# Performance work log

Hardware: AMD Instinct MI355X
Metric: run time of the kernel (lower is better)

## Reference

```python
import jax, jax.numpy as jnp
import numpy as np

D_DIST = 1.5       # init kwarg d_dist
NUM_LABELS = 64    # K; labels drawn from [0, K), all present w.h.p. at N=200k
B, C, N = 8, 32, 200000


def setup_inputs() -> dict:
    key = jax.random.key(0)
    k1, k2 = jax.random.split(key)
    prediction = jax.random.normal(k1, (B, C, N), dtype=jnp.float32)
    label = jax.random.randint(k2, (B, N), 0, NUM_LABELS)
    return {"prediction": prediction, "label": label}


def _batch_loss(pred, lab):
    # pred: [C, N], lab: [N] int in [0, K)
    K = NUM_LABELS
    counts = jax.ops.segment_sum(jnp.ones(lab.shape, pred.dtype), lab, num_segments=K)  # [K]
    sums = jax.ops.segment_sum(pred.T, lab, num_segments=K)                              # [K, C]
    center = sums / jnp.maximum(counts, 1.0)[:, None]                                    # [K, C] per-label mean
    # square_distance_single(center, center): pairwise sq-dist between the C columns
    # of center (coordinates are the K cluster axes) -> [C, C], exactly as the torch code.
    gram = center.T @ center                       # [C, C]
    n2 = jnp.sum(center * center, axis=0)          # [C]
    sq = jax.nn.relu(n2[:, None] + n2[None, :] - 2.0 * gram)
    # safe sqrt: identical forward to sqrt(relu(sq)) but finite grads at 0
    dist = jnp.where(sq > 0, jnp.sqrt(jnp.where(sq > 0, sq, 1.0)), 0.0)
    hinge = jax.nn.relu(2.0 * D_DIST - dist)
    return jnp.sum(hinge * hinge) / (2.0 * K * (K - 1.0 + 1e-16))


def reference(prediction, label):
    # sum over batches, matching the python loop accumulation
    return jnp.sum(jax.vmap(_batch_loss)(prediction, label))
```

## Files before the change

kernel.cpp:

```cpp
#include <hip/hip_runtime.h>
#include <stdint.h>

#define BATCH    8
#define CDIM     32
#define KLBL     64
#define NPB      200000
#define SLABS_PB 6250
#define CHUNKS   128
#define TSLAB    4
#define LROWB    272
#define TILEB    (32 * LROWB)

typedef __attribute__((ext_vector_type(8))) short bf16x8;
typedef __attribute__((ext_vector_type(4))) float f32x4;

union ABits { uint32_t u[4]; bf16x8 v; };

__device__ __forceinline__ uint32_t cvtpk_bf16(float lo, float hi) {
  uint32_t r;
  asm volatile("v_cvt_pk_bf16_f32 %0, %1, %2" : "=v"(r) : "v"(lo), "v"(hi));
  return r;
}

__global__ __launch_bounds__(256) void pack_kernel(
    const int* __restrict__ lab, uint8_t* __restrict__ lab8, int total4) {
  const int i = blockIdx.x * 256 + threadIdx.x;
  if (i < total4) {
    const int4 l4 = ((const int4*)lab)[i];
    ((uint32_t*)lab8)[i] = (uint32_t)(l4.x & 0xff) |
                           ((uint32_t)(l4.y & 0xff) << 8) |
                           ((uint32_t)(l4.z & 0xff) << 16) |
                           ((uint32_t)(l4.w & 0xff) << 24);
  }
}

__global__ __launch_bounds__(256) void seg_mfma_kernel(
    const float* __restrict__ pred,
    const uint8_t* __restrict__ lab8,
    float* __restrict__ gsums,
    float* __restrict__ gcounts) {
  __shared__ __align__(8)  uint32_t s_lab[400];
  __shared__ __align__(16) uint8_t  s_tile[2][TILEB];

  const int tid = threadIdx.x;
  const int wv = tid >> 6;
  const int ln = tid & 63;
  const int chunk = blockIdx.x, b = blockIdx.y;

  const int s0 = (int)((long long)chunk * SLABS_PB / CHUNKS);
  const int s1 = (int)((long long)(chunk + 1) * SLABS_PB / CHUNKS);
  const int nslab = s1 - s0;
  const int base_n = s0 * 32;

  const uint32_t* lsrc = (const uint32_t*)(lab8 + (size_t)b * NPB + base_n);
  for (int i = tid; i < nslab * 8; i += 256) s_lab[i] = lsrc[i];

  const float* rowp[4];
#pragma unroll
  for (int j = 0; j < 4; ++j) {
    const int c = wv * 8 + j * 2 + (ln >> 5);
    rowp[j] = pred + ((size_t)b * CDIM + c) * NPB;
  }
  const int lan4 = (ln & 31) * 4;

  ABits ones;
  ones.u[0] = ones.u[1] = ones.u[2] = ones.u[3] = 0x3F803F80u;

  f32x4 acc0 = {0.f, 0.f, 0.f, 0.f};
  f32x4 acc1 = {0.f, 0.f, 0.f, 0.f};
  f32x4 accc = {0.f, 0.f, 0.f, 0.f};

  const int ntile = (nslab + TSLAB - 1) / TSLAB;
  const uint32_t myrow = (uint32_t)((ln & 15) + (wv << 4));

  float4 r0, r1, r2, r3;

  auto issue_loads = [&](int t) {
    int en = base_n + t * 128 + lan4;
    en = min(en, NPB - 4);
    r0 = *(const float4*)(rowp[0] + en);
    r1 = *(const float4*)(rowp[1] + en);
    r2 = *(const float4*)(rowp[2] + en);
    r3 = *(const float4*)(rowp[3] + en);
  };

  auto cvt_write = [&](int buf) {
    uint8_t* tb = s_tile[buf];
    const int off = (ln & 31) * 8;
#pragma unroll
    for (int j = 0; j < 4; ++j) {
      const float4 r = (j == 0) ? r0 : (j == 1) ? r1 : (j == 2) ? r2 : r3;
      const int c = wv * 8 + j * 2 + (ln >> 5);
      uint2 w;
      w.x = cvtpk_bf16(r.x, r.y);
      w.y = cvtpk_bf16(r.z, r.w);
      *(uint2*)(tb + c * LROWB + off) = w;
    }
  };

  auto process = [&](int t, int buf) {
    const uint8_t* tb = s_tile[buf];
    const int ns = min(TSLAB, nslab - t * TSLAB);
    const int rb = (ln & 15) * LROWB + (ln >> 4) * 16;
    for (int ss = 0; ss < ns; ++ss) {
      const int sb = t * TSLAB + ss;
      const uint2 lw =
          *(const uint2*)((const uint8_t*)s_lab + sb * 32 + (ln >> 4) * 8);
      ABits a;
      a.u[0] = (((lw.x) & 0xffu) == myrow ? 0x3F80u : 0u) |
               (((lw.x >> 8) & 0xffu) == myrow ? 0x3F800000u : 0u);
      a.u[1] = (((lw.x >> 16) & 0xffu) == myrow ? 0x3F80u : 0u) |
               (((lw.x >> 24) & 0xffu) == myrow ? 0x3F800000u : 0u);
      a.u[2] = (((lw.y) & 0xffu) == myrow ? 0x3F80u : 0u) |
               (((lw.y >> 8) & 0xffu) == myrow ? 0x3F800000u : 0u);
      a.u[3] = (((lw.y >> 16) & 0xffu) == myrow ? 0x3F80u : 0u) |
               (((lw.y >> 24) & 0xffu) == myrow ? 0x3F800000u : 0u);
      const bf16x8 b0 = *(const bf16x8*)(tb + rb + ss * 64);
      const bf16x8 b1 = *(const bf16x8*)(tb + rb + ss * 64 + 16 * LROWB);
      acc0 = __builtin_amdgcn_mfma_f32_16x16x32_bf16(a.v, b0, acc0, 0, 0, 0);
      acc1 = __builtin_amdgcn_mfma_f32_16x16x32_bf16(a.v, b1, acc1, 0, 0, 0);
      accc = __builtin_amdgcn_mfma_f32_16x16x32_bf16(a.v, ones.v, accc, 0, 0, 0);
    }
  };

  issue_loads(0);
  cvt_write(0);
  __syncthreads();

  for (int t = 0; t < ntile; ++t) {
    const int buf = t & 1;
    const bool more = (t + 1 < ntile);
    if (more) issue_loads(t + 1);
    __builtin_amdgcn_sched_barrier(0);
    process(t, buf);
    if (more) cvt_write(buf ^ 1);
    __syncthreads();
  }

  const int krb = (wv << 4) + ((ln >> 4) << 2);
  const int col = ln & 15;
  float* gs = gsums + (size_t)b * KLBL * CDIM;
#pragma unroll
  for (int r = 0; r < 4; ++r) {
    atomicAdd(&gs[(krb + r) * CDIM + col], acc0[r]);
    atomicAdd(&gs[(krb + r) * CDIM + 16 + col], acc1[r]);
  }
  if (col == 0) {
#pragma unroll
    for (int r = 0; r < 4; ++r)
      atomicAdd(&gcounts[b * KLBL + krb + r], accc[r]);
  }
}

__global__ __launch_bounds__(256) void loss_kernel(
    const float* __restrict__ gsums,
    const float* __restrict__ gcounts,
    float* __restrict__ out) {
  const int b = blockIdx.x;
  __shared__ float s_center[KLBL * CDIM];
  __shared__ float s_red[256];

  for (int i = threadIdx.x; i < KLBL * CDIM; i += 256) {
    const float cnt = fmaxf(gcounts[b * KLBL + (i >> 5)], 1.0f);
    s_center[i] = gsums[(size_t)b * KLBL * CDIM + i] / cnt;
  }
  __syncthreads();

  float acc = 0.f;
  for (int p = threadIdx.x; p < CDIM * CDIM; p += 256) {
    const int i = p >> 5, j = p & 31;
    float g = 0.f, ni = 0.f, nj = 0.f;
#pragma unroll
    for (int k = 0; k < KLBL; ++k) {
      const float ci = s_center[k * CDIM + i];
      const float cj = s_center[k * CDIM + j];
      g += ci * cj;
      ni += ci * ci;
      nj += cj * cj;
    }
    float sq = fmaxf(ni + nj - 2.f * g, 0.f);
    const float dist = (sq > 0.f) ? sqrtf(sq) : 0.f;
    const float h = fmaxf(3.0f - dist, 0.f);
    acc += h * h;
  }

  s_red[threadIdx.x] = acc;
  __syncthreads();
  for (int s = 128; s > 0; s >>= 1) {
    if (threadIdx.x < s) s_red[threadIdx.x] += s_red[threadIdx.x + s];
    __syncthreads();
  }
  if (threadIdx.x == 0)
    atomicAdd(out, s_red[0] / (2.0f * (float)KLBL * ((float)KLBL - 1.0f)));
}

extern "C" void kernel_launch(void* const* d_in, const int* in_sizes, int n_in,
                              void* d_out, int out_size, void* d_ws, size_t ws_size,
                              hipStream_t stream) {
  const float* pred  = (const float*)d_in[0];
  const int*   label = (const int*)d_in[1];
  float* out = (float*)d_out;

  float*   gsums   = (float*)d_ws;
  float*   gcounts = gsums + (size_t)BATCH * KLBL * CDIM;
  uint8_t* lab8    = (uint8_t*)(gcounts + BATCH * KLBL);

  const size_t accum_bytes =
      (size_t)(BATCH * KLBL * CDIM + BATCH * KLBL) * sizeof(float);
  hipMemsetAsync(d_ws, 0, accum_bytes, stream);
  hipMemsetAsync(d_out, 0, sizeof(float), stream);

  const int total4 = BATCH * NPB / 4;
  pack_kernel<<<(total4 + 255) / 256, 256, 0, stream>>>(label, lab8, total4);

  dim3 grid1(CHUNKS, BATCH);
  seg_mfma_kernel<<<grid1, 256, 0, stream>>>(pred, lab8, gsums, gcounts);

  loss_kernel<<<BATCH, 256, 0, stream>>>(gsums, gcounts, out);
}
```

Baseline: 68.44 us.

## Fuse label packing into segment kernel and deepen prefetch to two tiles

```diff
diff --git a/kernel.cpp b/kernel.cpp
--- a/kernel.cpp
+++ b/kernel.cpp
@@ -22,21 +22,9 @@
   return r;
 }
 
-__global__ __launch_bounds__(256) void pack_kernel(
-    const int* __restrict__ lab, uint8_t* __restrict__ lab8, int total4) {
-  const int i = blockIdx.x * 256 + threadIdx.x;
-  if (i < total4) {
-    const int4 l4 = ((const int4*)lab)[i];
-    ((uint32_t*)lab8)[i] = (uint32_t)(l4.x & 0xff) |
-                           ((uint32_t)(l4.y & 0xff) << 8) |
-                           ((uint32_t)(l4.z & 0xff) << 16) |
-                           ((uint32_t)(l4.w & 0xff) << 24);
-  }
-}
-
 __global__ __launch_bounds__(256) void seg_mfma_kernel(
     const float* __restrict__ pred,
-    const uint8_t* __restrict__ lab8,
+    const int*   __restrict__ label,
     float* __restrict__ gsums,
     float* __restrict__ gcounts) {
   __shared__ __align__(8)  uint32_t s_lab[400];
@@ -52,8 +40,12 @@
   const int nslab = s1 - s0;
   const int base_n = s0 * 32;
 
-  const uint32_t* lsrc = (const uint32_t*)(lab8 + (size_t)b * NPB + base_n);
-  for (int i = tid; i < nslab * 8; i += 256) s_lab[i] = lsrc[i];
+  const int4* lsrc = (const int4*)(label + (size_t)b * NPB + base_n);
+  for (int i = tid; i < nslab * 8; i += 256) {
+    const int4 l4 = lsrc[i];
+    s_lab[i] = (uint32_t)(l4.x & 0xff) | ((uint32_t)(l4.y & 0xff) << 8) |
+               ((uint32_t)(l4.z & 0xff) << 16) | ((uint32_t)(l4.w & 0xff) << 24);
+  }
 
   const float* rowp[4];
 #pragma unroll
@@ -73,28 +65,47 @@
   const int ntile = (nslab + TSLAB - 1) / TSLAB;
   const uint32_t myrow = (uint32_t)((ln & 15) + (wv << 4));
 
-  float4 r0, r1, r2, r3;
-
-  auto issue_loads = [&](int t) {
-    int en = base_n + t * 128 + lan4;
-    en = min(en, NPB - 4);
-    r0 = *(const float4*)(rowp[0] + en);
-    r1 = *(const float4*)(rowp[1] + en);
-    r2 = *(const float4*)(rowp[2] + en);
-    r3 = *(const float4*)(rowp[3] + en);
-  };
-
-  auto cvt_write = [&](int buf) {
+  float4 rA0, rA1, rA2, rA3;
+  float4 rB0, rB1, rB2, rB3;
+
+  auto loadA = [&](int t) {
+    const int en = min(base_n + t * 128 + lan4, NPB - 4);
+    rA0 = *(const float4*)(rowp[0] + en);
+    rA1 = *(const float4*)(rowp[1] + en);
+    rA2 = *(const float4*)(rowp[2] + en);
+    rA3 = *(const float4*)(rowp[3] + en);
+  };
+  auto loadB = [&](int t) {
+    const int en = min(base_n + t * 128 + lan4, NPB - 4);
+    rB0 = *(const float4*)(rowp[0] + en);
+    rB1 = *(const float4*)(rowp[1] + en);
+    rB2 = *(const float4*)(rowp[2] + en);
+    rB3 = *(const float4*)(rowp[3] + en);
+  };
+
+  const int cvt_off = (ln & 31) * 8;
+  auto cvtA = [&](int buf) {
     uint8_t* tb = s_tile[buf];
-    const int off = (ln & 31) * 8;
 #pragma unroll
     for (int j = 0; j < 4; ++j) {
-      const float4 r = (j == 0) ? r0 : (j == 1) ? r1 : (j == 2) ? r2 : r3;
+      const float4 r = (j == 0) ? rA0 : (j == 1) ? rA1 : (j == 2) ? rA2 : rA3;
       const int c = wv * 8 + j * 2 + (ln >> 5);
       uint2 w;
       w.x = cvtpk_bf16(r.x, r.y);
       w.y = cvtpk_bf16(r.z, r.w);
-      *(uint2*)(tb + c * LROWB + off) = w;
+      *(uint2*)(tb + c * LROWB + cvt_off) = w;
+    }
+  };
+  auto cvtB = [&](int buf) {
+    uint8_t* tb = s_tile[buf];
+#pragma unroll
+    for (int j = 0; j < 4; ++j) {
+      const float4 r = (j == 0) ? rB0 : (j == 1) ? rB1 : (j == 2) ? rB2 : rB3;
+      const int c = wv * 8 + j * 2 + (ln >> 5);
+      uint2 w;
+      w.x = cvtpk_bf16(r.x, r.y);
+      w.y = cvtpk_bf16(r.z, r.w);
+      *(uint2*)(tb + c * LROWB + cvt_off) = w;
     }
   };
 
@@ -123,18 +134,26 @@
     }
   };
 
-  issue_loads(0);
-  cvt_write(0);
+  loadA(0);
+  if (ntile > 1) loadB(1);
+  cvtA(0);
   __syncthreads();
 
-  for (int t = 0; t < ntile; ++t) {
-    const int buf = t & 1;
-    const bool more = (t + 1 < ntile);
-    if (more) issue_loads(t + 1);
+  int t = 0;
+  while (t < ntile) {
+    if (t + 2 < ntile) loadA(t + 2);
     __builtin_amdgcn_sched_barrier(0);
-    process(t, buf);
-    if (more) cvt_write(buf ^ 1);
+    process(t, 0);
+    if (t + 1 < ntile) cvtB(1);
     __syncthreads();
+    ++t;
+    if (t >= ntile) break;
+    if (t + 2 < ntile) loadB(t + 2);
+    __builtin_amdgcn_sched_barrier(0);
+    process(t, 1);
+    if (t + 1 < ntile) cvtA(0);
+    __syncthreads();
+    ++t;
   }
 
   const int krb = (wv << 4) + ((ln >> 4) << 2);
@@ -201,20 +220,16 @@
   const int*   label = (const int*)d_in[1];
   float* out = (float*)d_out;
 
-  float*   gsums   = (float*)d_ws;
-  float*   gcounts = gsums + (size_t)BATCH * KLBL * CDIM;
-  uint8_t* lab8    = (uint8_t*)(gcounts + BATCH * KLBL);
+  float* gsums   = (float*)d_ws;
+  float* gcounts = gsums + (size_t)BATCH * KLBL * CDIM;
 
   const size_t accum_bytes =
       (size_t)(BATCH * KLBL * CDIM + BATCH * KLBL) * sizeof(float);
   hipMemsetAsync(d_ws, 0, accum_bytes, stream);
   hipMemsetAsync(d_out, 0, sizeof(float), stream);
 
-  const int total4 = BATCH * NPB / 4;
-  pack_kernel<<<(total4 + 255) / 256, 256, 0, stream>>>(label, lab8, total4);
-
   dim3 grid1(CHUNKS, BATCH);
-  seg_mfma_kernel<<<grid1, 256, 0, stream>>>(pred, lab8, gsums, gcounts);
+  seg_mfma_kernel<<<grid1, 256, 0, stream>>>(pred, label, gsums, gcounts);
 
   loss_kernel<<<BATCH, 256, 0, stream>>>(gsums, gcounts, out);
 }
```

After: 66.33 us. -3.1%, faster.

## Load pred and labels directly into MFMA registers, drop pack kernel and LDS tiles

Applied to the files above, without the earlier changes.

```diff
diff --git a/kernel.cpp b/kernel.cpp
--- a/kernel.cpp
+++ b/kernel.cpp
@@ -6,10 +6,7 @@
 #define KLBL     64
 #define NPB      200000
 #define SLABS_PB 6250
-#define CHUNKS   128
-#define TSLAB    4
-#define LROWB    272
-#define TILEB    (32 * LROWB)
+#define CHUNKS   96
 
 typedef __attribute__((ext_vector_type(8))) short bf16x8;
 typedef __attribute__((ext_vector_type(4))) float f32x4;
@@ -22,25 +19,12 @@
   return r;
 }
 
-__global__ __launch_bounds__(256) void pack_kernel(
-    const int* __restrict__ lab, uint8_t* __restrict__ lab8, int total4) {
-  const int i = blockIdx.x * 256 + threadIdx.x;
-  if (i < total4) {
-    const int4 l4 = ((const int4*)lab)[i];
-    ((uint32_t*)lab8)[i] = (uint32_t)(l4.x & 0xff) |
-                           ((uint32_t)(l4.y & 0xff) << 8) |
-                           ((uint32_t)(l4.z & 0xff) << 16) |
-                           ((uint32_t)(l4.w & 0xff) << 24);
-  }
-}
-
 __global__ __launch_bounds__(256) void seg_mfma_kernel(
     const float* __restrict__ pred,
-    const uint8_t* __restrict__ lab8,
+    const int*   __restrict__ label,
     float* __restrict__ gsums,
     float* __restrict__ gcounts) {
-  __shared__ __align__(8)  uint32_t s_lab[400];
-  __shared__ __align__(16) uint8_t  s_tile[2][TILEB];
+  __shared__ float s_part[4][KLBL * CDIM + KLBL];
 
   const int tid = threadIdx.x;
   const int wv = tid >> 6;
@@ -49,106 +33,116 @@
 
   const int s0 = (int)((long long)chunk * SLABS_PB / CHUNKS);
   const int s1 = (int)((long long)(chunk + 1) * SLABS_PB / CHUNKS);
-  const int nslab = s1 - s0;
-  const int base_n = s0 * 32;
-
-  const uint32_t* lsrc = (const uint32_t*)(lab8 + (size_t)b * NPB + base_n);
-  for (int i = tid; i < nslab * 8; i += 256) s_lab[i] = lsrc[i];
-
-  const float* rowp[4];
-#pragma unroll
-  for (int j = 0; j < 4; ++j) {
-    const int c = wv * 8 + j * 2 + (ln >> 5);
-    rowp[j] = pred + ((size_t)b * CDIM + c) * NPB;
-  }
-  const int lan4 = (ln & 31) * 4;
+  const int w0 = s0 + (int)((long long)(s1 - s0) * wv / 4);
+  const int w1 = s0 + (int)((long long)(s1 - s0) * (wv + 1) / 4);
+
+  const int crow = ln & 15;
+  const int kseg = (ln >> 4) * 8;
+
+  const float* row0 = pred + ((size_t)b * CDIM + crow) * NPB;
+  const float* row1 = pred + ((size_t)b * CDIM + crow + 16) * NPB;
+  const int*   labp = label + (size_t)b * NPB;
 
   ABits ones;
   ones.u[0] = ones.u[1] = ones.u[2] = ones.u[3] = 0x3F803F80u;
 
-  f32x4 acc0 = {0.f, 0.f, 0.f, 0.f};
-  f32x4 acc1 = {0.f, 0.f, 0.f, 0.f};
-  f32x4 accc = {0.f, 0.f, 0.f, 0.f};
-
-  const int ntile = (nslab + TSLAB - 1) / TSLAB;
-  const uint32_t myrow = (uint32_t)((ln & 15) + (wv << 4));
-
-  float4 r0, r1, r2, r3;
-
-  auto issue_loads = [&](int t) {
-    int en = base_n + t * 128 + lan4;
-    en = min(en, NPB - 4);
-    r0 = *(const float4*)(rowp[0] + en);
-    r1 = *(const float4*)(rowp[1] + en);
-    r2 = *(const float4*)(rowp[2] + en);
-    r3 = *(const float4*)(rowp[3] + en);
-  };
-
-  auto cvt_write = [&](int buf) {
-    uint8_t* tb = s_tile[buf];
-    const int off = (ln & 31) * 8;
-#pragma unroll
-    for (int j = 0; j < 4; ++j) {
-      const float4 r = (j == 0) ? r0 : (j == 1) ? r1 : (j == 2) ? r2 : r3;
-      const int c = wv * 8 + j * 2 + (ln >> 5);
-      uint2 w;
-      w.x = cvtpk_bf16(r.x, r.y);
-      w.y = cvtpk_bf16(r.z, r.w);
-      *(uint2*)(tb + c * LROWB + off) = w;
-    }
-  };
-
-  auto process = [&](int t, int buf) {
-    const uint8_t* tb = s_tile[buf];
-    const int ns = min(TSLAB, nslab - t * TSLAB);
-    const int rb = (ln & 15) * LROWB + (ln >> 4) * 16;
-    for (int ss = 0; ss < ns; ++ss) {
-      const int sb = t * TSLAB + ss;
-      const uint2 lw =
-          *(const uint2*)((const uint8_t*)s_lab + sb * 32 + (ln >> 4) * 8);
-      ABits a;
-      a.u[0] = (((lw.x) & 0xffu) == myrow ? 0x3F80u : 0u) |
-               (((lw.x >> 8) & 0xffu) == myrow ? 0x3F800000u : 0u);
-      a.u[1] = (((lw.x >> 16) & 0xffu) == myrow ? 0x3F80u : 0u) |
-               (((lw.x >> 24) & 0xffu) == myrow ? 0x3F800000u : 0u);
-      a.u[2] = (((lw.y) & 0xffu) == myrow ? 0x3F80u : 0u) |
-               (((lw.y >> 8) & 0xffu) == myrow ? 0x3F800000u : 0u);
-      a.u[3] = (((lw.y >> 16) & 0xffu) == myrow ? 0x3F80u : 0u) |
-               (((lw.y >> 24) & 0xffu) == myrow ? 0x3F800000u : 0u);
-      const bf16x8 b0 = *(const bf16x8*)(tb + rb + ss * 64);
-      const bf16x8 b1 = *(const bf16x8*)(tb + rb + ss * 64 + 16 * LROWB);
-      acc0 = __builtin_amdgcn_mfma_f32_16x16x32_bf16(a.v, b0, acc0, 0, 0, 0);
-      acc1 = __builtin_amdgcn_mfma_f32_16x16x32_bf16(a.v, b1, acc1, 0, 0, 0);
-      accc = __builtin_amdgcn_mfma_f32_16x16x32_bf16(a.v, ones.v, accc, 0, 0, 0);
-    }
-  };
-
-  issue_loads(0);
-  cvt_write(0);
+  f32x4 acc[4][2];
+  f32x4 accc[4];
+#pragma unroll
+  for (int kt = 0; kt < 4; ++kt) {
+    acc[kt][0] = (f32x4){0.f, 0.f, 0.f, 0.f};
+    acc[kt][1] = (f32x4){0.f, 0.f, 0.f, 0.f};
+    accc[kt]   = (f32x4){0.f, 0.f, 0.f, 0.f};
+  }
+
+  float4 fA0, fA1, fA2, fA3;  int4 lA0, lA1;
+  float4 fB0, fB1, fB2, fB3;  int4 lB0, lB1;
+
+  auto loadA = [&](int s) {
+    const int n0 = s * 32 + kseg;
+    fA0 = *(const float4*)(row0 + n0);
+    fA1 = *(const float4*)(row0 + n0 + 4);
+    fA2 = *(const float4*)(row1 + n0);
+    fA3 = *(const float4*)(row1 + n0 + 4);
+    lA0 = *(const int4*)(labp + n0);
+    lA1 = *(const int4*)(labp + n0 + 4);
+  };
+  auto loadB = [&](int s) {
+    const int n0 = s * 32 + kseg;
+    fB0 = *(const float4*)(row0 + n0);
+    fB1 = *(const float4*)(row0 + n0 + 4);
+    fB2 = *(const float4*)(row1 + n0);
+    fB3 = *(const float4*)(row1 + n0 + 4);
+    lB0 = *(const int4*)(labp + n0);
+    lB1 = *(const int4*)(labp + n0 + 4);
+  };
+
+  ABits b0v, b1v, av[4];
+
+  auto derive = [&](const float4& f0, const float4& f1, const float4& f2,
+                    const float4& f3, const int4& l0, const int4& l1) {
+    b0v.u[0] = cvtpk_bf16(f0.x, f0.y);
+    b0v.u[1] = cvtpk_bf16(f0.z, f0.w);
+    b0v.u[2] = cvtpk_bf16(f1.x, f1.y);
+    b0v.u[3] = cvtpk_bf16(f1.z, f1.w);
+    b1v.u[0] = cvtpk_bf16(f2.x, f2.y);
+    b1v.u[1] = cvtpk_bf16(f2.z, f2.w);
+    b1v.u[2] = cvtpk_bf16(f3.x, f3.y);
+    b1v.u[3] = cvtpk_bf16(f3.z, f3.w);
+#pragma unroll
+    for (int kt = 0; kt < 4; ++kt) {
+      const int tgt = kt * 16 + crow;
+      av[kt].u[0] = (l0.x == tgt ? 0x3F80u : 0u) | (l0.y == tgt ? 0x3F800000u : 0u);
+      av[kt].u[1] = (l0.z == tgt ? 0x3F80u : 0u) | (l0.w == tgt ? 0x3F800000u : 0u);
+      av[kt].u[2] = (l1.x == tgt ? 0x3F80u : 0u) | (l1.y == tgt ? 0x3F800000u : 0u);
+      av[kt].u[3] = (l1.z == tgt ? 0x3F80u : 0u) | (l1.w == tgt ? 0x3F800000u : 0u);
+    }
+  };
+
+  auto mfma_step = [&]() {
+#pragma unroll
+    for (int kt = 0; kt < 4; ++kt) {
+      acc[kt][0] = __builtin_amdgcn_mfma_f32_16x16x32_bf16(av[kt].v, b0v.v, acc[kt][0], 0, 0, 0);
+      acc[kt][1] = __builtin_amdgcn_mfma_f32_16x16x32_bf16(av[kt].v, b1v.v, acc[kt][1], 0, 0, 0);
+      accc[kt]   = __builtin_amdgcn_mfma_f32_16x16x32_bf16(av[kt].v, ones.v, accc[kt], 0, 0, 0);
+    }
+  };
+
+  if (w0 < w1) loadA(w0);
+  if (w0 + 1 < w1) loadB(w0 + 1);
+
+  int s = w0;
+  while (s < w1) {
+    derive(fA0, fA1, fA2, fA3, lA0, lA1);
+    if (s + 2 < w1) loadA(s + 2);
+    __builtin_amdgcn_sched_barrier(0);
+    mfma_step();
+    ++s;
+    if (s >= w1) break;
+    derive(fB0, fB1, fB2, fB3, lB0, lB1);
+    if (s + 2 < w1) loadB(s + 2);
+    __builtin_amdgcn_sched_barrier(0);
+    mfma_step();
+    ++s;
+  }
+
+#pragma unroll
+  for (int kt = 0; kt < 4; ++kt) {
+#pragma unroll
+    for (int r = 0; r < 4; ++r) {
+      const int k = kt * 16 + (ln >> 4) * 4 + r;
+      s_part[wv][k * CDIM + crow]      = acc[kt][0][r];
+      s_part[wv][k * CDIM + 16 + crow] = acc[kt][1][r];
+      if (crow == 0) s_part[wv][KLBL * CDIM + k] = accc[kt][r];
+    }
+  }
   __syncthreads();
 
-  for (int t = 0; t < ntile; ++t) {
-    const int buf = t & 1;
-    const bool more = (t + 1 < ntile);
-    if (more) issue_loads(t + 1);
-    __builtin_amdgcn_sched_barrier(0);
-    process(t, buf);
-    if (more) cvt_write(buf ^ 1);
-    __syncthreads();
-  }
-
-  const int krb = (wv << 4) + ((ln >> 4) << 2);
-  const int col = ln & 15;
   float* gs = gsums + (size_t)b * KLBL * CDIM;
-#pragma unroll
-  for (int r = 0; r < 4; ++r) {
-    atomicAdd(&gs[(krb + r) * CDIM + col], acc0[r]);
-    atomicAdd(&gs[(krb + r) * CDIM + 16 + col], acc1[r]);
-  }
-  if (col == 0) {
-#pragma unroll
-    for (int r = 0; r < 4; ++r)
-      atomicAdd(&gcounts[b * KLBL + krb + r], accc[r]);
+  for (int i = tid; i < KLBL * CDIM + KLBL; i += 256) {
+    const float v = s_part[0][i] + s_part[1][i] + s_part[2][i] + s_part[3][i];
+    if (i < KLBL * CDIM) atomicAdd(&gs[i], v);
+    else                 atomicAdd(&gcounts[b * KLBL + (i - KLBL * CDIM)], v);
   }
 }
 
@@ -201,20 +195,16 @@
   const int*   label = (const int*)d_in[1];
   float* out = (float*)d_out;
 
-  float*   gsums   = (float*)d_ws;
-  float*   gcounts = gsums + (size_t)BATCH * KLBL * CDIM;
-  uint8_t* lab8    = (uint8_t*)(gcounts + BATCH * KLBL);
+  float* gsums   = (float*)d_ws;
+  float* gcounts = gsums + (size_t)BATCH * KLBL * CDIM;
 
   const size_t accum_bytes =
       (size_t)(BATCH * KLBL * CDIM + BATCH * KLBL) * sizeof(float);
   hipMemsetAsync(d_ws, 0, accum_bytes, stream);
   hipMemsetAsync(d_out, 0, sizeof(float), stream);
 
-  const int total4 = BATCH * NPB / 4;
-  pack_kernel<<<(total4 + 255) / 256, 256, 0, stream>>>(label, lab8, total4);
-
   dim3 grid1(CHUNKS, BATCH);
-  seg_mfma_kernel<<<grid1, 256, 0, stream>>>(pred, lab8, gsums, gcounts);
+  seg_mfma_kernel<<<grid1, 256, 0, stream>>>(pred, label, gsums, gcounts);
 
   loss_kernel<<<BATCH, 256, 0, stream>>>(gsums, gcounts, out);
 }
```

New measurement: 65.39 us. 1.05x faster.
